# Performance work log

Hardware: AMD Instinct MI355X
Metric: run time of the kernel (lower is better)

Reference implementation:

```python
import jax, jax.numpy as jnp
import numpy as np

# Sizes matching init_kwargs: r=2, J=3 -> K = 1 + (r-1)*J = 4 framelet operators
N, FEAT, K, NNZ = 20000, 64, 4, 320000
NU, GAMMA, J = 2.0, 1.0, 3  # nu, gamma_0 (gamma never updated on this code path)


def setup_inputs() -> dict:
    key = jax.random.key(0)
    ks = jax.random.split(key, 6)
    F = jax.random.normal(ks[0], (N, FEAT), dtype=jnp.float32)
    w_rows = jax.random.randint(ks[1], (K, NNZ), 0, N, dtype=jnp.int32)
    w_cols = jax.random.randint(ks[2], (K, NNZ), 0, N, dtype=jnp.int32)
    # scale ~1/avg_degree so the 14-step fixed-point iteration is contractive/stable
    w_vals = jax.random.normal(ks[3], (K, NNZ), dtype=jnp.float32) / 16.0
    d = jax.random.uniform(ks[4], (N,), dtype=jnp.float32)
    mask = jax.random.uniform(ks[5], (N, 1), dtype=jnp.float32)
    return {"F": F, "w_rows": w_rows, "w_cols": w_cols, "w_vals": w_vals,
            "d": d, "mask": mask, "thres_iter": 15}


def _spmm(rows, cols, vals, X):
    # sparse [N,N] @ dense [N,FEAT] via gather + segment-sum scatter
    return jax.ops.segment_sum(vals[:, None] * X[cols], rows, num_segments=N)


_spmm_shared = jax.vmap(_spmm, in_axes=(0, 0, 0, None))  # K operators, one dense X
_spmm_each = jax.vmap(_spmm, in_axes=(0, 0, 0, 0))       # K operators, K dense Xs


def _soft(x, thr):  # elementwise soft-thresholding: relu(x-t) - relu(-x-t)
    return jax.nn.relu(x - thr) - jax.nn.relu(-x - thr)


def reference(F, w_rows, w_cols, w_vals, d, mask, thres_iter):
    # nu_jl = [0] + [nu / 4^i for i in range(J)]
    nu = jnp.asarray([0.0] + [NU / (4.0 ** i) for i in range(J)], dtype=jnp.float32)  # [K]
    thr = (nu / GAMMA)[:, None, None] * d[None, :, None]  # [K,N,1] per-operator row thresholds
    d1 = d[:, None]                 # [N,1]
    m2 = mask * mask                # [N,1]
    denom = d1 * m2 + GAMMA         # [N,1]
    num_f = d1 * F * m2             # [N,FEAT]
    Y0 = jnp.zeros((K, N, FEAT), dtype=F.dtype)

    def step(carry, _):
        Uk, Y = carry
        # Z(k+1): soft-threshold of W_jl @ Uk + Y_jl / gamma
        Z = _soft(_spmm_shared(w_rows, w_cols, w_vals, Uk) + Y / GAMMA, thr)  # [K,N,FEAT]
        v = Y - GAMMA * Z
        WTV = _spmm_each(w_rows, w_cols, w_vals, v).sum(axis=0)               # [N,FEAT]
        Uk = (num_f - WTV) / denom
        # Y(k+1) dual update
        Y = Y + GAMMA * (_spmm_shared(w_rows, w_cols, w_vals, Uk) - Z)
        return (Uk, Y), None

    n_iter = int(thres_iter) - 1  # while k < thres_iter starting at k=1
    (Uk, _), _ = jax.lax.scan(jax.checkpoint(step), (F, Y0), None, length=n_iter)
    return Uk
```

## Files before the change

### kernel.cpp

```cpp
#include <hip/hip_runtime.h>


constexpr int N_    = 20000;
constexpr int FEAT_ = 64;
constexpr int K_    = 4;
constexpr int NNZ_  = 320000;
constexpr int NF    = N_ * FEAT_;
constexpr int KN    = K_ * N_;
constexpr int NEDGE = K_ * NNZ_;
constexpr int NITER = 14;
constexpr int BLK   = 256;
constexpr int NSB   = (KN + 255) / 256;
constexpr int NCPY  = 8;
constexpr int NXCD  = 8;
constexpr int EPV   = 2048;
constexpr int NVB   = NEDGE / EPV;

constexpr int R_SP  = 10;
constexpr int NB_SP = ((KN + R_SP - 1) / R_SP + 3) / 4;
constexpr int R_WT  = 4;
constexpr int NB_WT = ((N_ + R_WT - 1) / R_WT + 3) / 4;

__constant__ float c_nu[4] = {0.0f, 2.0f, 0.5f, 0.125f};

__device__ __forceinline__ float softf(float x, float t) {
    float a = fabsf(x) - t;
    a = a > 0.0f ? a : 0.0f;
    return copysignf(a, x);
}

__device__ __forceinline__ float bf2f(unsigned short u) {
    union { unsigned int i; float f; } x;
    x.i = ((unsigned int)u) << 16;
    return x.f;
}
__device__ __forceinline__ unsigned short f2bf(float f) {
    union { float f; unsigned int i; } x;
    x.f = f;
    unsigned int r = x.i + 0x7FFFu + ((x.i >> 16) & 1u);
    return (unsigned short)(r >> 16);
}

__device__ __forceinline__ void decode_meta(unsigned int p, int& c, float& v) {
    c = (int)((p >> 15) & 3u) * N_ + (int)(p & 0x7FFFu);
    unsigned int e5 = (p >> 26) & 0x1Fu;
    unsigned int bits = (p & 0x80000000u) | ((e5 + 96u) << 23) |
                        (((p >> 17) & 0x1FFu) << 14);
    v = (e5 == 0u) ? 0.0f : __uint_as_float(bits);
}


__global__ __launch_bounds__(BLK) void precompute_kernel(
    const float* __restrict__ F, const float* __restrict__ d,
    const float* __restrict__ mask, float* __restrict__ dm,
    unsigned short* __restrict__ F_bf) {
    int i = blockIdx.x * BLK + threadIdx.x;
    if (i >= NF / 4) return;
    float4 f = ((const float4*)F)[i];
    ushort4 o;
    o.x = f2bf(f.x); o.y = f2bf(f.y); o.z = f2bf(f.z); o.w = f2bf(f.w);
    ((ushort4*)F_bf)[i] = o;
    if ((i & (FEAT_ / 4 - 1)) == 0) {
        int n = i / (FEAT_ / 4);
        dm[n] = d[n] * mask[n] * mask[n];
    }
}

__global__ __launch_bounds__(BLK) void hist_kernel(
    const int* __restrict__ rows, int* __restrict__ cnt8) {
    int e = blockIdx.x * BLK + threadIdx.x;
    if (e >= NEDGE) return;
    int k = e / NNZ_;
    int copy = blockIdx.x & (NCPY - 1);
    atomicAdd(&cnt8[copy * KN + rows[e] * K_ + k], 1);
}

__global__ __launch_bounds__(256) void scan1_kernel(
    const int* __restrict__ cnt8, int* __restrict__ loc,
    int* __restrict__ bsum) {
    int i = blockIdx.x * 256 + threadIdx.x;
    int x = 0;
    if (i < KN) {
        #pragma unroll
        for (int c = 0; c < NCPY; ++c) x += cnt8[c * KN + i];
    }
    int lane = threadIdx.x & 63, wid = threadIdx.x >> 6;
    int v = x;
    #pragma unroll
    for (int off = 1; off < 64; off <<= 1) {
        int t = __shfl_up(v, off, 64);
        if (lane >= off) v += t;
    }
    __shared__ int ws[4];
    if (lane == 63) ws[wid] = v;
    __syncthreads();
    int add = 0;
    for (int u = 0; u < wid; ++u) add += ws[u];
    v += add;
    if (i < KN) loc[i] = v - x;
    if (threadIdx.x == 255) bsum[blockIdx.x] = v;
}

__global__ __launch_bounds__(512) void scan2_kernel(int* __restrict__ bsum) {
    int tid = threadIdx.x;
    int x = (tid < NSB) ? bsum[tid] : 0;
    int lane = tid & 63, wid = tid >> 6;
    int v = x;
    #pragma unroll
    for (int off = 1; off < 64; off <<= 1) {
        int t = __shfl_up(v, off, 64);
        if (lane >= off) v += t;
    }
    __shared__ int ws[8];
    if (lane == 63) ws[wid] = v;
    __syncthreads();
    int add = 0;
    for (int u = 0; u < wid; ++u) add += ws[u];
    v += add;
    if (tid < NSB) bsum[tid] = v - x;
}

__global__ __launch_bounds__(256) void scan3_kernel(
    const int* __restrict__ loc, const int* __restrict__ bsum,
    int* __restrict__ offs, int* __restrict__ cursor) {
    int i = blockIdx.x * 256 + threadIdx.x;
    if (i < KN) {
        int v = loc[i] + bsum[blockIdx.x];
        offs[i] = v;
        cursor[i] = v;
    }
    if (i == 0) offs[KN] = NEDGE;
}

__global__ __launch_bounds__(BLK) void scatter_kernel(
    const int* __restrict__ rows, const int* __restrict__ cols,
    const float* __restrict__ vals, int* __restrict__ cursor,
    unsigned int* __restrict__ cmeta) {
    int xcd = blockIdx.x & (NXCD - 1);
    int vb  = blockIdx.x >> 3;
    int ebase = vb * EPV;
    #pragma unroll
    for (int i = 0; i < EPV / BLK; ++i) {
        int e = ebase + i * BLK + threadIdx.x;
        int row = rows[e];
        if (row / (N_ / NXCD) != xcd) continue;
        int k = e / NNZ_;
        unsigned int b  = __float_as_uint(vals[e]);
        unsigned int rb = b + 0x1FFFu + ((b >> 14) & 1u);
        int exp8 = (int)((rb >> 23) & 0xFF);
        unsigned int pk = 0u;
        if (exp8 > 96)
            pk = (b & 0x80000000u) | ((unsigned int)(exp8 - 96) << 26) |
                 (((rb >> 14) & 0x1FFu) << 17);
        pk |= ((unsigned int)k << 15) | (unsigned int)cols[e];
        int pos = atomicAdd(&cursor[row * K_ + k], 1);
        cmeta[pos] = pk;
    }
}


template <int BATCH>
__device__ __forceinline__ void chunk_accum(
    int c_l, float v_l, int n, const ushort4* __restrict__ Xb,
    int sub, int q, float4& acc) {
    int iters = (n + 3) >> 2;
    int itersPad = (iters + BATCH - 1) & ~(BATCH - 1);
    for (int it0 = 0; it0 < itersPad; it0 += BATCH) {
        float   vv[BATCH];
        ushort4 xx[BATCH];
        #pragma unroll
        for (int u = 0; u < BATCH; ++u) {
            int j = 4 * (it0 + u) + sub;
            int   c = __shfl(c_l, j, 64);
            vv[u]   = __shfl(v_l, j, 64);
            xx[u]   = Xb[c * (FEAT_ / 4) + q];
        }
        #pragma unroll
        for (int u = 0; u < BATCH; ++u) {
            acc.x += vv[u] * bf2f(xx[u].x);
            acc.y += vv[u] * bf2f(xx[u].y);
            acc.z += vv[u] * bf2f(xx[u].z);
            acc.w += vv[u] * bf2f(xx[u].w);
        }
    }
}

template <int BATCH>
__device__ __forceinline__ void tail_accum(
    const unsigned int* __restrict__ cmeta, const ushort4* __restrict__ Xb,
    int beg, int end, int lane, int sub, int q, int padc, float4& acc) {
    for (int eb = beg; eb < end; eb += 64) {
        int n = end - eb;
        if (n > 64) n = 64;
        int   c_l = padc;
        float v_l = 0.0f;
        if (lane < n) {
            unsigned int p = cmeta[eb + lane];
            decode_meta(p, c_l, v_l);
        }
        chunk_accum<BATCH>(c_l, v_l, n, Xb, sub, q, acc);
    }
}

__device__ __forceinline__ void butterfly4(float4& a) {
    #pragma unroll
    for (int m = 16; m <= 32; m <<= 1) {
        a.x += __shfl_xor(a.x, m, 64);
        a.y += __shfl_xor(a.y, m, 64);
        a.z += __shfl_xor(a.z, m, 64);
        a.w += __shfl_xor(a.w, m, 64);
    }
}

template <bool FIRST>
__global__ __launch_bounds__(BLK) void spmm_fused_kernel(
    const int* __restrict__ offs, const unsigned int* __restrict__ cmeta,
    const unsigned short* __restrict__ Xb,
    const float* __restrict__ d, unsigned short* __restrict__ V_bf) {
    int wave = (blockIdx.x * BLK + threadIdx.x) >> 6;
    int lane = threadIdx.x & 63;
    int sub  = lane >> 4, q = lane & 15;
    int base = wave * R_SP;
    if (base >= KN) return;
    int off_l = 0;
    if (lane <= R_SP) {
        int i = base + lane;
        if (i > KN) i = KN;
        off_l = offs[i];
    }
    const ushort4* X4 = (const ushort4*)Xb;
    ushort4* V4 = (ushort4*)V_bf;

    unsigned int p_cur = 0u;
    {
        int b0 = __shfl(off_l, 0, 64), e0 = __shfl(off_l, 1, 64);
        int nn = e0 - b0;
        if (nn > 64) nn = 64;
        if (lane < nn) p_cur = cmeta[b0 + lane];
    }
    for (int r = 0; r < R_SP; ++r) {
        int w = base + r;
        if (w >= KN) break;
        int k = w & (K_ - 1);
        int n = w >> 2;
        int beg = __shfl(off_l, r, 64);
        int end = __shfl(off_l, r + 1, 64);
        unsigned int p_nxt = 0u;
        if (r + 1 < R_SP && w + 1 < KN) {
            int bn = __shfl(off_l, r + 1, 64), en = __shfl(off_l, r + 2, 64);
            int nn = en - bn;
            if (nn > 64) nn = 64;
            if (lane < nn) p_nxt = cmeta[bn + lane];
        }
        int n_e = end - beg;
        if (n_e > 64) n_e = 64;
        int   c_l = k * N_;
        float v_l = 0.0f;
        if (lane < n_e) decode_meta(p_cur, c_l, v_l);
        const ushort4* X4m = X4 - (size_t)k * N_ * (FEAT_ / 4);
        float4 acc = {0.f, 0.f, 0.f, 0.f};
        chunk_accum<4>(c_l, v_l, n_e, X4m, sub, q, acc);
        if (end - beg > 64)
            tail_accum<4>(cmeta, X4m, beg + 64, end, lane, sub, q, k * N_, acc);
        p_cur = p_nxt;
        butterfly4(acc);
        if (sub == 0) {
            int idx4 = (k * N_ + n) * (FEAT_ / 4) + q;
            float thr = c_nu[k] * d[n];
            float4 y;
            if (FIRST) {
                y = make_float4(0.f, 0.f, 0.f, 0.f);
            } else {
                ushort4 vp = V4[idx4];
                y.x = acc.x + bf2f(vp.x); y.y = acc.y + bf2f(vp.y);
                y.z = acc.z + bf2f(vp.z); y.w = acc.w + bf2f(vp.w);
            }
            ushort4 o;
            o.x = f2bf(y.x - softf(acc.x + y.x, thr));
            o.y = f2bf(y.y - softf(acc.y + y.y, thr));
            o.z = f2bf(y.z - softf(acc.z + y.z, thr));
            o.w = f2bf(y.w - softf(acc.w + y.w, thr));
            V4[idx4] = o;
        }
    }
}

__global__ __launch_bounds__(BLK) void wtv_u_kernel(
    const int* __restrict__ offs, const unsigned int* __restrict__ cmeta,
    const unsigned short* __restrict__ V_bf,
    const float* __restrict__ F, const float* __restrict__ dm,
    float* __restrict__ U, unsigned short* __restrict__ U_bf) {
    int wave = (blockIdx.x * BLK + threadIdx.x) >> 6;
    int lane = threadIdx.x & 63;
    int sub  = lane >> 4, q = lane & 15;
    int base = wave * R_WT;
    if (base >= N_) return;
    int off_l = 0;
    if (lane <= K_ * R_WT) {
        int i = K_ * base + lane;
        if (i > KN) i = KN;
        off_l = offs[i];
    }
    const ushort4* V4 = (const ushort4*)V_bf;

    unsigned int p0 = 0u, p1 = 0u;
    {
        int b0 = __shfl(off_l, 0, 64), e0 = __shfl(off_l, K_, 64);
        int nn = e0 - b0;
        if (lane < nn) p0 = cmeta[b0 + lane];
        if (64 + lane < nn) p1 = cmeta[b0 + 64 + lane];
    }
    for (int r = 0; r < R_WT; ++r) {
        int n = base + r;
        if (n >= N_) break;
        int beg = __shfl(off_l, K_ * r, 64);
        int end = __shfl(off_l, K_ * r + K_, 64);
        unsigned int q0 = 0u, q1 = 0u;
        if (r + 1 < R_WT && n + 1 < N_) {
            int bn = __shfl(off_l, K_ * r + K_, 64);
            int en = __shfl(off_l, K_ * r + 2 * K_, 64);
            int nn = en - bn;
            if (lane < nn) q0 = cmeta[bn + lane];
            if (64 + lane < nn) q1 = cmeta[bn + 64 + lane];
        }
        int ne = end - beg;
        float4 acc = {0.f, 0.f, 0.f, 0.f};
        {
            int n0 = ne > 64 ? 64 : ne;
            int   c_l = 0;
            float v_l = 0.0f;
            if (lane < n0) decode_meta(p0, c_l, v_l);
            chunk_accum<8>(c_l, v_l, n0, V4, sub, q, acc);
        }
        if (ne > 64) {
            int n1 = ne - 64;
            if (n1 > 64) n1 = 64;
            int   c_l = 0;
            float v_l = 0.0f;
            if (lane < n1) decode_meta(p1, c_l, v_l);
            chunk_accum<2>(c_l, v_l, n1, V4, sub, q, acc);
        }
        if (ne > 128)
            tail_accum<2>(cmeta, V4, beg + 128, end, lane, sub, q, 0, acc);
        p0 = q0; p1 = q1;
        butterfly4(acc);
        if (sub == 0) {
            int idx4 = n * (FEAT_ / 4) + q;
            float dmv = dm[n];
            float r2 = 1.0f / (dmv + 1.0f);
            float4 f = ((const float4*)F)[idx4];
            float4 o;
            o.x = (dmv * f.x - acc.x) * r2; o.y = (dmv * f.y - acc.y) * r2;
            o.z = (dmv * f.z - acc.z) * r2; o.w = (dmv * f.w - acc.w) * r2;
            ((float4*)U)[idx4] = o;
            ushort4 ob;
            ob.x = f2bf(o.x); ob.y = f2bf(o.y);
            ob.z = f2bf(o.z); ob.w = f2bf(o.w);
            ((ushort4*)U_bf)[idx4] = ob;
        }
    }
}

extern "C" void kernel_launch(void* const* d_in, const int* in_sizes, int n_in,
                              void* d_out, int out_size, void* d_ws, size_t ws_size,
                              hipStream_t stream) {
    const float* F      = (const float*)d_in[0];
    const int*   w_rows = (const int*)d_in[1];
    const int*   w_cols = (const int*)d_in[2];
    const float* w_vals = (const float*)d_in[3];
    const float* d      = (const float*)d_in[4];
    const float* mask   = (const float*)d_in[5];
    float* U = (float*)d_out;

    unsigned int* cmeta  = (unsigned int*)d_ws;
    unsigned short* V_bf = (unsigned short*)(cmeta + NEDGE);
    unsigned short* U_bf = V_bf + (size_t)KN * FEAT_;
    unsigned short* F_bf = U_bf + NF;
    float* dm     = (float*)(F_bf + NF);
    int*   cnt8   = (int*)(dm + N_);
    int*   loc    = cnt8 + NCPY * KN;
    int*   bsum   = loc + KN;
    int*   offs   = bsum + 512;
    int*   cursor = offs + KN + 1;

    const int gEdge = NEDGE / BLK;
    const int gNF4  = (NF / 4) / BLK;

    hipMemsetAsync(cnt8, 0, (size_t)NCPY * KN * 4, stream);
    precompute_kernel<<<gNF4, BLK, 0, stream>>>(F, d, mask, dm, F_bf);
    hist_kernel<<<gEdge, BLK, 0, stream>>>(w_rows, cnt8);
    scan1_kernel<<<NSB, 256, 0, stream>>>(cnt8, loc, bsum);
    scan2_kernel<<<1, 512, 0, stream>>>(bsum);
    scan3_kernel<<<NSB, 256, 0, stream>>>(loc, bsum, offs, cursor);
    scatter_kernel<<<NVB * NXCD, BLK, 0, stream>>>(w_rows, w_cols, w_vals,
                                                   cursor, cmeta);

    spmm_fused_kernel<true><<<NB_SP, BLK, 0, stream>>>(offs, cmeta, F_bf, d, V_bf);
    for (int it = 0; it < NITER; ++it) {
        wtv_u_kernel<<<NB_WT, BLK, 0, stream>>>(offs, cmeta, V_bf,
                                                F, dm, U, U_bf);
        if (it < NITER - 1)
            spmm_fused_kernel<false><<<NB_SP, BLK, 0, stream>>>(offs, cmeta,
                                                                U_bf, d, V_bf);
    }
}
```

Baseline: 907.0 us.

## Prefetch next row's gathered features across row loop; skip fp32 U writes until last

Both SpMM kernels now decode the next row's metadata and issue its first batch of feature gathers before the current row's reduction and epilogue run, so gather latency overlaps with the shuffle reduction and stores. The wtv kernel is templated so the fp32 U output is written only on the final iteration, since intermediate iterations read only the bf16 copy. The extra prefetch buffers (up to 16 ushort4 plus floats per lane) raise register pressure, which may lower occupancy.

```diff
diff --git a/kernel.cpp b/kernel.cpp
--- a/kernel.cpp
+++ b/kernel.cpp
@@ -47,6 +47,13 @@
     unsigned int bits = (p & 0x80000000u) | ((e5 + 96u) << 23) |
                         (((p >> 17) & 0x1FFu) << 14);
     v = (e5 == 0u) ? 0.0f : __uint_as_float(bits);
+}
+
+__device__ __forceinline__ void fma4(float4& acc, float v, const ushort4& x) {
+    acc.x += v * bf2f(x.x);
+    acc.y += v * bf2f(x.y);
+    acc.z += v * bf2f(x.z);
+    acc.w += v * bf2f(x.w);
 }
 
 
@@ -160,28 +167,22 @@
 
 
 template <int BATCH>
-__device__ __forceinline__ void chunk_accum(
-    int c_l, float v_l, int n, const ushort4* __restrict__ Xb,
+__device__ __forceinline__ void accum_from(
+    int c_l, float v_l, int n, int it_start, const ushort4* __restrict__ Xb,
     int sub, int q, float4& acc) {
     int iters = (n + 3) >> 2;
-    int itersPad = (iters + BATCH - 1) & ~(BATCH - 1);
-    for (int it0 = 0; it0 < itersPad; it0 += BATCH) {
+    for (int it0 = it_start; it0 < iters; it0 += BATCH) {
         float   vv[BATCH];
         ushort4 xx[BATCH];
         #pragma unroll
         for (int u = 0; u < BATCH; ++u) {
             int j = 4 * (it0 + u) + sub;
-            int   c = __shfl(c_l, j, 64);
-            vv[u]   = __shfl(v_l, j, 64);
-            xx[u]   = Xb[c * (FEAT_ / 4) + q];
-        }
-        #pragma unroll
-        for (int u = 0; u < BATCH; ++u) {
-            acc.x += vv[u] * bf2f(xx[u].x);
-            acc.y += vv[u] * bf2f(xx[u].y);
-            acc.z += vv[u] * bf2f(xx[u].z);
-            acc.w += vv[u] * bf2f(xx[u].w);
-        }
+            int c = __shfl(c_l, j, 64);
+            vv[u] = __shfl(v_l, j, 64);
+            xx[u] = Xb[(size_t)c * (FEAT_ / 4) + q];
+        }
+        #pragma unroll
+        for (int u = 0; u < BATCH; ++u) fma4(acc, vv[u], xx[u]);
     }
 }
 
@@ -198,7 +199,7 @@
             unsigned int p = cmeta[eb + lane];
             decode_meta(p, c_l, v_l);
         }
-        chunk_accum<BATCH>(c_l, v_l, n, Xb, sub, q, acc);
+        accum_from<BATCH>(c_l, v_l, n, 0, Xb, sub, q, acc);
     }
 }
 
@@ -231,13 +232,33 @@
     const ushort4* X4 = (const ushort4*)Xb;
     ushort4* V4 = (ushort4*)V_bf;
 
-    unsigned int p_cur = 0u;
+    int   cC = 0; float vC = 0.0f; int nC = 0;
+    ushort4 xx[4]; float vv[4];
+    unsigned int p_nxt = 0u;
+
     {
         int b0 = __shfl(off_l, 0, 64), e0 = __shfl(off_l, 1, 64);
-        int nn = e0 - b0;
-        if (nn > 64) nn = 64;
-        if (lane < nn) p_cur = cmeta[b0 + lane];
-    }
+        nC = e0 - b0; if (nC > 64) nC = 64;
+        int k0 = base & (K_ - 1);
+        unsigned int p = 0u;
+        if (lane < nC) p = cmeta[b0 + lane];
+        cC = k0 * N_; vC = 0.0f;
+        if (lane < nC) decode_meta(p, cC, vC);
+        const ushort4* Xm = X4 - (size_t)k0 * N_ * (FEAT_ / 4);
+        #pragma unroll
+        for (int u = 0; u < 4; ++u) {
+            int j = 4 * u + sub;
+            int c = __shfl(cC, j, 64);
+            vv[u] = __shfl(vC, j, 64);
+            xx[u] = Xm[(size_t)c * (FEAT_ / 4) + q];
+        }
+        if (base + 1 < KN) {
+            int b1 = e0, e1 = __shfl(off_l, 2, 64);
+            int nn = e1 - b1; if (nn > 64) nn = 64;
+            if (lane < nn) p_nxt = cmeta[b1 + lane];
+        }
+    }
+
     for (int r = 0; r < R_SP; ++r) {
         int w = base + r;
         if (w >= KN) break;
@@ -245,24 +266,36 @@
         int n = w >> 2;
         int beg = __shfl(off_l, r, 64);
         int end = __shfl(off_l, r + 1, 64);
-        unsigned int p_nxt = 0u;
+        int n_e = nC;
+        const ushort4* Xm = X4 - (size_t)k * N_ * (FEAT_ / 4);
+        float4 acc = {0.f, 0.f, 0.f, 0.f};
+        #pragma unroll
+        for (int u = 0; u < 4; ++u) fma4(acc, vv[u], xx[u]);
+        if (n_e > 16)
+            accum_from<4>(cC, vC, n_e, 4, Xm, sub, q, acc);
+        if (end - beg > 64)
+            tail_accum<4>(cmeta, Xm, beg + 64, end, lane, sub, q, k * N_, acc);
         if (r + 1 < R_SP && w + 1 < KN) {
-            int bn = __shfl(off_l, r + 1, 64), en = __shfl(off_l, r + 2, 64);
-            int nn = en - bn;
-            if (nn > 64) nn = 64;
-            if (lane < nn) p_nxt = cmeta[bn + lane];
-        }
-        int n_e = end - beg;
-        if (n_e > 64) n_e = 64;
-        int   c_l = k * N_;
-        float v_l = 0.0f;
-        if (lane < n_e) decode_meta(p_cur, c_l, v_l);
-        const ushort4* X4m = X4 - (size_t)k * N_ * (FEAT_ / 4);
-        float4 acc = {0.f, 0.f, 0.f, 0.f};
-        chunk_accum<4>(c_l, v_l, n_e, X4m, sub, q, acc);
-        if (end - beg > 64)
-            tail_accum<4>(cmeta, X4m, beg + 64, end, lane, sub, q, k * N_, acc);
-        p_cur = p_nxt;
+            int bn = end, en = __shfl(off_l, r + 2, 64);
+            nC = en - bn; if (nC > 64) nC = 64;
+            int kn = (w + 1) & (K_ - 1);
+            cC = kn * N_; vC = 0.0f;
+            if (lane < nC) decode_meta(p_nxt, cC, vC);
+            const ushort4* Xn = X4 - (size_t)kn * N_ * (FEAT_ / 4);
+            #pragma unroll
+            for (int u = 0; u < 4; ++u) {
+                int j = 4 * u + sub;
+                int c = __shfl(cC, j, 64);
+                vv[u] = __shfl(vC, j, 64);
+                xx[u] = Xn[(size_t)c * (FEAT_ / 4) + q];
+            }
+            p_nxt = 0u;
+            if (r + 2 < R_SP && w + 2 < KN) {
+                int b2 = en, e2 = __shfl(off_l, r + 3, 64);
+                int nn = e2 - b2; if (nn > 64) nn = 64;
+                if (lane < nn) p_nxt = cmeta[b2 + lane];
+            }
+        }
         butterfly4(acc);
         if (sub == 0) {
             int idx4 = (k * N_ + n) * (FEAT_ / 4) + q;
@@ -285,6 +318,7 @@
     }
 }
 
+template <bool LAST>
 __global__ __launch_bounds__(BLK) void wtv_u_kernel(
     const int* __restrict__ offs, const unsigned int* __restrict__ cmeta,
     const unsigned short* __restrict__ V_bf,
@@ -303,46 +337,100 @@
     }
     const ushort4* V4 = (const ushort4*)V_bf;
 
-    unsigned int p0 = 0u, p1 = 0u;
+    int c0 = 0, c1 = 0; float v0 = 0.0f, v1 = 0.0f; int neC = 0;
+    ushort4 xx[16]; float vv[16];
+    unsigned int q0 = 0u, q1 = 0u;
+
     {
         int b0 = __shfl(off_l, 0, 64), e0 = __shfl(off_l, K_, 64);
-        int nn = e0 - b0;
-        if (lane < nn) p0 = cmeta[b0 + lane];
-        if (64 + lane < nn) p1 = cmeta[b0 + 64 + lane];
-    }
+        neC = e0 - b0;
+        unsigned int p0 = 0u, p1 = 0u;
+        if (lane < neC) p0 = cmeta[b0 + lane];
+        if (64 + lane < neC) p1 = cmeta[b0 + 64 + lane];
+        int n0 = neC > 64 ? 64 : neC;
+        if (lane < n0) decode_meta(p0, c0, v0);
+        if (neC > 64) {
+            int n1 = neC - 64; if (n1 > 64) n1 = 64;
+            if (lane < n1) decode_meta(p1, c1, v1);
+        }
+        #pragma unroll
+        for (int u = 0; u < 8; ++u) {
+            int j = 4 * u + sub;
+            int c = __shfl(c0, j, 64);
+            vv[u] = __shfl(v0, j, 64);
+            xx[u] = V4[(size_t)c * (FEAT_ / 4) + q];
+        }
+        if (n0 > 32) {
+            #pragma unroll
+            for (int u = 8; u < 16; ++u) {
+                int j = 4 * u + sub;
+                int c = __shfl(c0, j, 64);
+                vv[u] = __shfl(v0, j, 64);
+                xx[u] = V4[(size_t)c * (FEAT_ / 4) + q];
+            }
+        }
+        if (base + 1 < N_) {
+            int bn = e0, en = __shfl(off_l, 2 * K_, 64);
+            int nn = en - bn;
+            if (lane < nn) q0 = cmeta[bn + lane];
+            if (64 + lane < nn) q1 = cmeta[bn + 64 + lane];
+        }
+    }
+
     for (int r = 0; r < R_WT; ++r) {
         int n = base + r;
         if (n >= N_) break;
         int beg = __shfl(off_l, K_ * r, 64);
         int end = __shfl(off_l, K_ * r + K_, 64);
-        unsigned int q0 = 0u, q1 = 0u;
-        if (r + 1 < R_WT && n + 1 < N_) {
-            int bn = __shfl(off_l, K_ * r + K_, 64);
-            int en = __shfl(off_l, K_ * r + 2 * K_, 64);
-            int nn = en - bn;
-            if (lane < nn) q0 = cmeta[bn + lane];
-            if (64 + lane < nn) q1 = cmeta[bn + 64 + lane];
-        }
-        int ne = end - beg;
+        int ne = neC;
+        int n0 = ne > 64 ? 64 : ne;
         float4 acc = {0.f, 0.f, 0.f, 0.f};
-        {
-            int n0 = ne > 64 ? 64 : ne;
-            int   c_l = 0;
-            float v_l = 0.0f;
-            if (lane < n0) decode_meta(p0, c_l, v_l);
-            chunk_accum<8>(c_l, v_l, n0, V4, sub, q, acc);
+        #pragma unroll
+        for (int u = 0; u < 8; ++u) fma4(acc, vv[u], xx[u]);
+        if (n0 > 32) {
+            #pragma unroll
+            for (int u = 8; u < 16; ++u) fma4(acc, vv[u], xx[u]);
         }
         if (ne > 64) {
-            int n1 = ne - 64;
-            if (n1 > 64) n1 = 64;
-            int   c_l = 0;
-            float v_l = 0.0f;
-            if (lane < n1) decode_meta(p1, c_l, v_l);
-            chunk_accum<2>(c_l, v_l, n1, V4, sub, q, acc);
+            int n1 = ne - 64; if (n1 > 64) n1 = 64;
+            accum_from<2>(c1, v1, n1, 0, V4, sub, q, acc);
         }
         if (ne > 128)
             tail_accum<2>(cmeta, V4, beg + 128, end, lane, sub, q, 0, acc);
-        p0 = q0; p1 = q1;
+        if (r + 1 < R_WT && n + 1 < N_) {
+            int bn = end, en = __shfl(off_l, K_ * r + 2 * K_, 64);
+            neC = en - bn;
+            int n0n = neC > 64 ? 64 : neC;
+            c0 = 0; v0 = 0.0f; c1 = 0; v1 = 0.0f;
+            if (lane < n0n) decode_meta(q0, c0, v0);
+            if (neC > 64) {
+                int n1n = neC - 64; if (n1n > 64) n1n = 64;
+                if (lane < n1n) decode_meta(q1, c1, v1);
+            }
+            #pragma unroll
+            for (int u = 0; u < 8; ++u) {
+                int j = 4 * u + sub;
+                int c = __shfl(c0, j, 64);
+                vv[u] = __shfl(v0, j, 64);
+                xx[u] = V4[(size_t)c * (FEAT_ / 4) + q];
+            }
+            if (n0n > 32) {
+                #pragma unroll
+                for (int u = 8; u < 16; ++u) {
+                    int j = 4 * u + sub;
+                    int c = __shfl(c0, j, 64);
+                    vv[u] = __shfl(v0, j, 64);
+                    xx[u] = V4[(size_t)c * (FEAT_ / 4) + q];
+                }
+            }
+            q0 = 0u; q1 = 0u;
+            if (r + 2 < R_WT && n + 2 < N_) {
+                int b2 = en, e2 = __shfl(off_l, K_ * r + 3 * K_, 64);
+                int nn = e2 - b2;
+                if (lane < nn) q0 = cmeta[b2 + lane];
+                if (64 + lane < nn) q1 = cmeta[b2 + 64 + lane];
+            }
+        }
         butterfly4(acc);
         if (sub == 0) {
             int idx4 = n * (FEAT_ / 4) + q;
@@ -352,7 +440,7 @@
             float4 o;
             o.x = (dmv * f.x - acc.x) * r2; o.y = (dmv * f.y - acc.y) * r2;
             o.z = (dmv * f.z - acc.z) * r2; o.w = (dmv * f.w - acc.w) * r2;
-            ((float4*)U)[idx4] = o;
+            if (LAST) ((float4*)U)[idx4] = o;
             ushort4 ob;
             ob.x = f2bf(o.x); ob.y = f2bf(o.y);
             ob.z = f2bf(o.z); ob.w = f2bf(o.w);
@@ -397,10 +485,14 @@
 
     spmm_fused_kernel<true><<<NB_SP, BLK, 0, stream>>>(offs, cmeta, F_bf, d, V_bf);
     for (int it = 0; it < NITER; ++it) {
-        wtv_u_kernel<<<NB_WT, BLK, 0, stream>>>(offs, cmeta, V_bf,
-                                                F, dm, U, U_bf);
-        if (it < NITER - 1)
+        if (it < NITER - 1) {
+            wtv_u_kernel<false><<<NB_WT, BLK, 0, stream>>>(offs, cmeta, V_bf,
+                                                           F, dm, U, U_bf);
             spmm_fused_kernel<false><<<NB_SP, BLK, 0, stream>>>(offs, cmeta,
                                                                 U_bf, d, V_bf);
-    }
-}
+        } else {
+            wtv_u_kernel<true><<<NB_WT, BLK, 0, stream>>>(offs, cmeta, V_bf,
+                                                          F, dm, U, U_bf);
+        }
+    }
+}
```

Result: slower. 945.9 us (+4.3%).

## Stage edges into per-XCD buckets during histogram and skip intermediate fp32 U writes

Applied to the files above, without the earlier changes.

The histogram kernel now also packs each edge's value, column and operator index and writes it into one of eight row-range buckets, using block-local counters plus one global atomic per bucket. The scatter pass then reads only its own bucket instead of having every XCD scan all edges and discard seven eighths of them. The bucket staging area reuses the V_bf buffer, which is free until the first SpMM. Separately, the fp32 U output is written only on the last iteration, since earlier iterations use only the bf16 copy. The bucket capacity is fixed at 81*2048 entries per bucket, so a skewed row distribution could overflow it.

```diff
diff --git a/kernel.cpp b/kernel.cpp
--- a/kernel.cpp
+++ b/kernel.cpp
@@ -13,8 +13,10 @@
 constexpr int NSB   = (KN + 255) / 256;
 constexpr int NCPY  = 8;
 constexpr int NXCD  = 8;
+constexpr int NPB   = N_ / NXCD;
 constexpr int EPV   = 2048;
-constexpr int NVB   = NEDGE / EPV;
+constexpr int CAP   = 81 * EPV;
+constexpr int NCH   = CAP / EPV;
 
 constexpr int R_SP  = 10;
 constexpr int NB_SP = ((KN + R_SP - 1) / R_SP + 3) / 4;
@@ -47,6 +49,17 @@
     unsigned int bits = (p & 0x80000000u) | ((e5 + 96u) << 23) |
                         (((p >> 17) & 0x1FFu) << 14);
     v = (e5 == 0u) ? 0.0f : __uint_as_float(bits);
+}
+
+__device__ __forceinline__ unsigned int pack_val(float val) {
+    unsigned int b  = __float_as_uint(val);
+    unsigned int rb = b + 0x1FFFu + ((b >> 14) & 1u);
+    int exp8 = (int)((rb >> 23) & 0xFF);
+    unsigned int pk = 0u;
+    if (exp8 > 96)
+        pk = (b & 0x80000000u) | ((unsigned int)(exp8 - 96) << 26) |
+             (((rb >> 14) & 0x1FFu) << 17);
+    return pk;
 }
 
 
@@ -66,13 +79,34 @@
     }
 }
 
-__global__ __launch_bounds__(BLK) void hist_kernel(
-    const int* __restrict__ rows, int* __restrict__ cnt8) {
+__global__ __launch_bounds__(BLK) void hist_stage_kernel(
+    const int* __restrict__ rows, const int* __restrict__ cols,
+    const float* __restrict__ vals, int* __restrict__ cnt8,
+    int* __restrict__ bcur, unsigned int* __restrict__ stage_pk,
+    unsigned short* __restrict__ stage_rk) {
+    __shared__ int lcnt[NXCD];
+    __shared__ int lbase[NXCD];
     int e = blockIdx.x * BLK + threadIdx.x;
-    if (e >= NEDGE) return;
+    if (threadIdx.x < NXCD) lcnt[threadIdx.x] = 0;
+    __syncthreads();
+    int row = rows[e];
+    int col = cols[e];
+    float val = vals[e];
     int k = e / NNZ_;
     int copy = blockIdx.x & (NCPY - 1);
-    atomicAdd(&cnt8[copy * KN + rows[e] * K_ + k], 1);
+    atomicAdd(&cnt8[copy * KN + row * K_ + k], 1);
+    int bkt = row / NPB;
+    int r_loc = atomicAdd(&lcnt[bkt], 1);
+    unsigned int pk = pack_val(val) | ((unsigned int)k << 15) |
+                      (unsigned int)col;
+    unsigned short rk16 = (unsigned short)((row - bkt * NPB) * K_ + k);
+    __syncthreads();
+    if (threadIdx.x < NXCD)
+        lbase[threadIdx.x] = atomicAdd(&bcur[threadIdx.x], lcnt[threadIdx.x]);
+    __syncthreads();
+    int pos = bkt * CAP + lbase[bkt] + r_loc;
+    stage_pk[pos] = pk;
+    stage_rk[pos] = rk16;
 }
 
 __global__ __launch_bounds__(256) void scan1_kernel(
@@ -132,28 +166,23 @@
     if (i == 0) offs[KN] = NEDGE;
 }
 
-__global__ __launch_bounds__(BLK) void scatter_kernel(
-    const int* __restrict__ rows, const int* __restrict__ cols,
-    const float* __restrict__ vals, int* __restrict__ cursor,
+__global__ __launch_bounds__(BLK) void scatter2_kernel(
+    const unsigned int* __restrict__ stage_pk,
+    const unsigned short* __restrict__ stage_rk,
+    const int* __restrict__ bcur, int* __restrict__ cursor,
     unsigned int* __restrict__ cmeta) {
-    int xcd = blockIdx.x & (NXCD - 1);
-    int vb  = blockIdx.x >> 3;
-    int ebase = vb * EPV;
+    int bkt   = blockIdx.x & (NXCD - 1);
+    int chunk = blockIdx.x >> 3;
+    int cnt   = bcur[bkt];
+    int base  = chunk * EPV + threadIdx.x;
+    int rkb   = bkt * NPB * K_;
     #pragma unroll
     for (int i = 0; i < EPV / BLK; ++i) {
-        int e = ebase + i * BLK + threadIdx.x;
-        int row = rows[e];
-        if (row / (N_ / NXCD) != xcd) continue;
-        int k = e / NNZ_;
-        unsigned int b  = __float_as_uint(vals[e]);
-        unsigned int rb = b + 0x1FFFu + ((b >> 14) & 1u);
-        int exp8 = (int)((rb >> 23) & 0xFF);
-        unsigned int pk = 0u;
-        if (exp8 > 96)
-            pk = (b & 0x80000000u) | ((unsigned int)(exp8 - 96) << 26) |
-                 (((rb >> 14) & 0x1FFu) << 17);
-        pk |= ((unsigned int)k << 15) | (unsigned int)cols[e];
-        int pos = atomicAdd(&cursor[row * K_ + k], 1);
+        int idx = base + i * BLK;
+        if (idx >= cnt) continue;
+        unsigned int pk = stage_pk[bkt * CAP + idx];
+        int rk = rkb + (int)stage_rk[bkt * CAP + idx];
+        int pos = atomicAdd(&cursor[rk], 1);
         cmeta[pos] = pk;
     }
 }
@@ -285,6 +314,7 @@
     }
 }
 
+template <bool LAST>
 __global__ __launch_bounds__(BLK) void wtv_u_kernel(
     const int* __restrict__ offs, const unsigned int* __restrict__ cmeta,
     const unsigned short* __restrict__ V_bf,
@@ -352,7 +382,7 @@
             float4 o;
             o.x = (dmv * f.x - acc.x) * r2; o.y = (dmv * f.y - acc.y) * r2;
             o.z = (dmv * f.z - acc.z) * r2; o.w = (dmv * f.w - acc.w) * r2;
-            ((float4*)U)[idx4] = o;
+            if (LAST) ((float4*)U)[idx4] = o;
             ushort4 ob;
             ob.x = f2bf(o.x); ob.y = f2bf(o.y);
             ob.z = f2bf(o.z); ob.w = f2bf(o.w);
@@ -378,29 +408,37 @@
     unsigned short* F_bf = U_bf + NF;
     float* dm     = (float*)(F_bf + NF);
     int*   cnt8   = (int*)(dm + N_);
-    int*   loc    = cnt8 + NCPY * KN;
+    int*   bcur   = cnt8 + NCPY * KN;
+    int*   loc    = bcur + NXCD;
     int*   bsum   = loc + KN;
     int*   offs   = bsum + 512;
     int*   cursor = offs + KN + 1;
+    unsigned int*   stage_pk = (unsigned int*)V_bf;
+    unsigned short* stage_rk = (unsigned short*)(stage_pk + NXCD * CAP);
 
     const int gEdge = NEDGE / BLK;
     const int gNF4  = (NF / 4) / BLK;
 
-    hipMemsetAsync(cnt8, 0, (size_t)NCPY * KN * 4, stream);
+    hipMemsetAsync(cnt8, 0, ((size_t)NCPY * KN + NXCD) * 4, stream);
     precompute_kernel<<<gNF4, BLK, 0, stream>>>(F, d, mask, dm, F_bf);
-    hist_kernel<<<gEdge, BLK, 0, stream>>>(w_rows, cnt8);
+    hist_stage_kernel<<<gEdge, BLK, 0, stream>>>(w_rows, w_cols, w_vals,
+                                                 cnt8, bcur, stage_pk, stage_rk);
     scan1_kernel<<<NSB, 256, 0, stream>>>(cnt8, loc, bsum);
     scan2_kernel<<<1, 512, 0, stream>>>(bsum);
     scan3_kernel<<<NSB, 256, 0, stream>>>(loc, bsum, offs, cursor);
-    scatter_kernel<<<NVB * NXCD, BLK, 0, stream>>>(w_rows, w_cols, w_vals,
-                                                   cursor, cmeta);
+    scatter2_kernel<<<NCH * NXCD, BLK, 0, stream>>>(stage_pk, stage_rk,
+                                                    bcur, cursor, cmeta);
 
     spmm_fused_kernel<true><<<NB_SP, BLK, 0, stream>>>(offs, cmeta, F_bf, d, V_bf);
     for (int it = 0; it < NITER; ++it) {
-        wtv_u_kernel<<<NB_WT, BLK, 0, stream>>>(offs, cmeta, V_bf,
-                                                F, dm, U, U_bf);
-        if (it < NITER - 1)
+        if (it < NITER - 1) {
+            wtv_u_kernel<false><<<NB_WT, BLK, 0, stream>>>(offs, cmeta, V_bf,
+                                                           F, dm, U, U_bf);
             spmm_fused_kernel<false><<<NB_SP, BLK, 0, stream>>>(offs, cmeta,
                                                                 U_bf, d, V_bf);
-    }
-}
+        } else {
+            wtv_u_kernel<true><<<NB_WT, BLK, 0, stream>>>(offs, cmeta, V_bf,
+                                                          F, dm, U, U_bf);
+        }
+    }
+}
```

New measurement: 923.9 us. No clear change (+1.9%).

## Restructure SpMM so each wave handles whole rows with K-operators split across subgroups

Applied to the files above, without the earlier changes.

Each wave in the SpMM kernel now processes three rows at a time. Each 16-lane subgroup handles one of the four framelet operators, replacing the old scheme of ten (row, operator) segments per wave with cross-subgroup reduction. Edge metadata for a row is decoded into an LDS table, padded to avoid bank conflicts, and each subgroup gathers four neighbours per step. This removes the butterfly reductions and improves memory-level parallelism. The fp32 U output is now written only on the final iteration. Overflow beyond 192 edges per row falls back to a serial slow path, and the extra LDS use may limit occupancy.

```diff
diff --git a/kernel.cpp b/kernel.cpp
--- a/kernel.cpp
+++ b/kernel.cpp
@@ -16,8 +16,11 @@
 constexpr int EPV   = 2048;
 constexpr int NVB   = NEDGE / EPV;
 
-constexpr int R_SP  = 10;
-constexpr int NB_SP = ((KN + R_SP - 1) / R_SP + 3) / 4;
+constexpr int T_SP  = 3;
+constexpr int NW_SP = (N_ + T_SP - 1) / T_SP;
+constexpr int NB_SP4 = (NW_SP + 3) / 4;
+constexpr int TABSZ = 204;
+
 constexpr int R_WT  = 4;
 constexpr int NB_WT = ((N_ + R_WT - 1) / R_WT + 3) / 4;
 
@@ -47,6 +50,22 @@
     unsigned int bits = (p & 0x80000000u) | ((e5 + 96u) << 23) |
                         (((p >> 17) & 0x1FFu) << 14);
     v = (e5 == 0u) ? 0.0f : __uint_as_float(bits);
+}
+
+__device__ __forceinline__ unsigned long long enc_tab(unsigned int p) {
+    unsigned int c16 = (p & 0x7FFFu) << 4;
+    unsigned int e5 = (p >> 26) & 0x1Fu;
+    unsigned int vb = (p & 0x80000000u) | ((e5 + 96u) << 23) |
+                      (((p >> 17) & 0x1FFu) << 14);
+    vb = (e5 == 0u) ? 0u : vb;
+    return ((unsigned long long)vb << 32) | (unsigned long long)c16;
+}
+
+__device__ __forceinline__ void fma4(float4& acc, float v, const ushort4& x) {
+    acc.x += v * bf2f(x.x);
+    acc.y += v * bf2f(x.y);
+    acc.z += v * bf2f(x.z);
+    acc.w += v * bf2f(x.w);
 }
 
 
@@ -217,56 +236,92 @@
     const int* __restrict__ offs, const unsigned int* __restrict__ cmeta,
     const unsigned short* __restrict__ Xb,
     const float* __restrict__ d, unsigned short* __restrict__ V_bf) {
+    __shared__ unsigned long long tab[4][2][TABSZ];
     int wave = (blockIdx.x * BLK + threadIdx.x) >> 6;
     int lane = threadIdx.x & 63;
     int sub  = lane >> 4, q = lane & 15;
-    int base = wave * R_SP;
-    if (base >= KN) return;
+    int widx = threadIdx.x >> 6;
+    int n0 = wave * T_SP;
+    if (n0 >= N_) return;
     int off_l = 0;
-    if (lane <= R_SP) {
-        int i = base + lane;
+    if (lane <= 4 * T_SP) {
+        int i = n0 * K_ + lane;
         if (i > KN) i = KN;
         off_l = offs[i];
     }
     const ushort4* X4 = (const ushort4*)Xb;
     ushort4* V4 = (ushort4*)V_bf;
-
-    unsigned int p_cur = 0u;
-    {
-        int b0 = __shfl(off_l, 0, 64), e0 = __shfl(off_l, 1, 64);
-        int nn = e0 - b0;
-        if (nn > 64) nn = 64;
-        if (lane < nn) p_cur = cmeta[b0 + lane];
-    }
-    for (int r = 0; r < R_SP; ++r) {
-        int w = base + r;
-        if (w >= KN) break;
-        int k = w & (K_ - 1);
-        int n = w >> 2;
-        int beg = __shfl(off_l, r, 64);
-        int end = __shfl(off_l, r + 1, 64);
-        unsigned int p_nxt = 0u;
-        if (r + 1 < R_SP && w + 1 < KN) {
-            int bn = __shfl(off_l, r + 1, 64), en = __shfl(off_l, r + 2, 64);
-            int nn = en - bn;
-            if (nn > 64) nn = 64;
-            if (lane < nn) p_nxt = cmeta[bn + lane];
-        }
-        int n_e = end - beg;
-        if (n_e > 64) n_e = 64;
-        int   c_l = k * N_;
-        float v_l = 0.0f;
-        if (lane < n_e) decode_meta(p_cur, c_l, v_l);
-        const ushort4* X4m = X4 - (size_t)k * N_ * (FEAT_ / 4);
+    float nu_s = sub == 0 ? 0.0f : (sub == 1 ? 2.0f : (sub == 2 ? 0.5f : 0.125f));
+
+    int tb = __shfl(off_l, 0, 64);
+    int te = __shfl(off_l, 4, 64);
+    int span = te - tb;
+    unsigned int pA = 0, pB = 0, pC = 0;
+    if (lane < span)       pA = cmeta[tb + lane];
+    if (64 + lane < span)  pB = cmeta[tb + 64 + lane];
+    if (128 + lane < span) pC = cmeta[tb + 128 + lane];
+
+    #pragma unroll
+    for (int t = 0; t < T_SP; ++t) {
+        int n = n0 + t;
+        if (n >= N_) break;
+        unsigned long long* Tc = tab[widx][t & 1];
+        int bs = __shfl(off_l, 4 * t + sub, 64);
+        int es = __shfl(off_l, 4 * t + sub + 1, 64);
+        int pre = bs - tb;
+        int cnt = es - bs;
+        int jmax = 192 - pre;
+        jmax = cnt < jmax ? cnt : jmax;
+        if (jmax < 0) jmax = 0;
+        int maxc = jmax;
+        { int o1 = __shfl_xor(maxc, 16, 64); maxc = maxc > o1 ? maxc : o1;
+          int o2 = __shfl_xor(maxc, 32, 64); maxc = maxc > o2 ? maxc : o2; }
+        if (lane < span)       { int s = lane;       Tc[s + (s >> 4)] = enc_tab(pA); }
+        if (64 + lane < span)  { int s = 64 + lane;  Tc[s + (s >> 4)] = enc_tab(pB); }
+        if (128 + lane < span) { int s = 128 + lane; Tc[s + (s >> 4)] = enc_tab(pC); }
+        int tbn = te, ten = te, spann = 0;
+        unsigned int nA = 0, nB = 0, nC = 0;
+        if (t + 1 < T_SP && n + 1 < N_) {
+            ten = __shfl(off_l, 4 * t + 8, 64);
+            spann = ten - tbn;
+            if (lane < spann)       nA = cmeta[tbn + lane];
+            if (64 + lane < spann)  nB = cmeta[tbn + 64 + lane];
+            if (128 + lane < spann) nC = cmeta[tbn + 128 + lane];
+        }
+        asm volatile("s_waitcnt lgkmcnt(0)" ::: "memory");
         float4 acc = {0.f, 0.f, 0.f, 0.f};
-        chunk_accum<4>(c_l, v_l, n_e, X4m, sub, q, acc);
-        if (end - beg > 64)
-            tail_accum<4>(cmeta, X4m, beg + 64, end, lane, sub, q, k * N_, acc);
-        p_cur = p_nxt;
-        butterfly4(acc);
-        if (sub == 0) {
-            int idx4 = (k * N_ + n) * (FEAT_ / 4) + q;
-            float thr = c_nu[k] * d[n];
+        for (int i0 = 0; i0 < maxc; i0 += 4) {
+            float vv[4]; int cc[4];
+            #pragma unroll
+            for (int u = 0; u < 4; ++u) {
+                int j = i0 + u;
+                bool ok = j < jmax;
+                int slot = ok ? pre + j : 0;
+                unsigned long long e = Tc[slot + (slot >> 4)];
+                cc[u] = (int)(unsigned int)e;
+                vv[u] = ok ? __uint_as_float((unsigned int)(e >> 32)) : 0.0f;
+            }
+            ushort4 xx[4];
+            #pragma unroll
+            for (int u = 0; u < 4; ++u) xx[u] = X4[cc[u] + q];
+            #pragma unroll
+            for (int u = 0; u < 4; ++u) fma4(acc, vv[u], xx[u]);
+        }
+        if (span > 192) {
+            for (int e = tb + 192; e < te; ++e) {
+                unsigned int p = cmeta[e];
+                int ke = (int)((p >> 15) & 3u);
+                unsigned long long en = enc_tab(p);
+                if (sub == ke) {
+                    ushort4 x = X4[(int)(unsigned int)en + q];
+                    fma4(acc, __uint_as_float((unsigned int)(en >> 32)), x);
+                }
+            }
+        }
+        {
+            float dn = d[n];
+            int idx4 = (sub * N_ + n) * (FEAT_ / 4) + q;
+            float thr = nu_s * dn;
             float4 y;
             if (FIRST) {
                 y = make_float4(0.f, 0.f, 0.f, 0.f);
@@ -282,9 +337,12 @@
             o.w = f2bf(y.w - softf(acc.w + y.w, thr));
             V4[idx4] = o;
         }
-    }
-}
-
+        tb = tbn; te = ten; span = spann;
+        pA = nA; pB = nB; pC = nC;
+    }
+}
+
+template <bool LAST>
 __global__ __launch_bounds__(BLK) void wtv_u_kernel(
     const int* __restrict__ offs, const unsigned int* __restrict__ cmeta,
     const unsigned short* __restrict__ V_bf,
@@ -326,11 +384,11 @@
         int ne = end - beg;
         float4 acc = {0.f, 0.f, 0.f, 0.f};
         {
-            int n0 = ne > 64 ? 64 : ne;
+            int n0c = ne > 64 ? 64 : ne;
             int   c_l = 0;
             float v_l = 0.0f;
-            if (lane < n0) decode_meta(p0, c_l, v_l);
-            chunk_accum<8>(c_l, v_l, n0, V4, sub, q, acc);
+            if (lane < n0c) decode_meta(p0, c_l, v_l);
+            chunk_accum<8>(c_l, v_l, n0c, V4, sub, q, acc);
         }
         if (ne > 64) {
             int n1 = ne - 64;
@@ -352,7 +410,7 @@
             float4 o;
             o.x = (dmv * f.x - acc.x) * r2; o.y = (dmv * f.y - acc.y) * r2;
             o.z = (dmv * f.z - acc.z) * r2; o.w = (dmv * f.w - acc.w) * r2;
-            ((float4*)U)[idx4] = o;
+            if (LAST) ((float4*)U)[idx4] = o;
             ushort4 ob;
             ob.x = f2bf(o.x); ob.y = f2bf(o.y);
             ob.z = f2bf(o.z); ob.w = f2bf(o.w);
@@ -395,12 +453,16 @@
     scatter_kernel<<<NVB * NXCD, BLK, 0, stream>>>(w_rows, w_cols, w_vals,
                                                    cursor, cmeta);
 
-    spmm_fused_kernel<true><<<NB_SP, BLK, 0, stream>>>(offs, cmeta, F_bf, d, V_bf);
+    spmm_fused_kernel<true><<<NB_SP4, BLK, 0, stream>>>(offs, cmeta, F_bf, d, V_bf);
     for (int it = 0; it < NITER; ++it) {
-        wtv_u_kernel<<<NB_WT, BLK, 0, stream>>>(offs, cmeta, V_bf,
-                                                F, dm, U, U_bf);
-        if (it < NITER - 1)
-            spmm_fused_kernel<false><<<NB_SP, BLK, 0, stream>>>(offs, cmeta,
-                                                                U_bf, d, V_bf);
-    }
-}
+        if (it < NITER - 1) {
+            wtv_u_kernel<false><<<NB_WT, BLK, 0, stream>>>(offs, cmeta, V_bf,
+                                                           F, dm, U, U_bf);
+            spmm_fused_kernel<false><<<NB_SP4, BLK, 0, stream>>>(offs, cmeta,
+                                                                 U_bf, d, V_bf);
+        } else {
+            wtv_u_kernel<true><<<NB_WT, BLK, 0, stream>>>(offs, cmeta, V_bf,
+                                                          F, dm, U, U_bf);
+        }
+    }
+}
```

New measurement: 817.5 us. -9.9%, faster.
